# Performance work log

Measured on AMD Instinct MI355X. Metric: run time of the kernel, lower is better.

The kernel has to match this reference:

```python
import jax, jax.numpy as jnp
import numpy as np

C = 768; NUM_HEADS = 12; HID = 3072
HP = 14; WP = 14; TF = 8; BATCH = 4
EPS = 1e-5


def layer_norm(x, g, b):
    mu = jnp.mean(x, axis=-1, keepdims=True)
    var = jnp.mean((x - mu) ** 2, axis=-1, keepdims=True)
    return (x - mu) / jnp.sqrt(var + EPS) * g + b


def mha(x, qkv_w, qkv_b, proj_w, proj_b):
    # Manual multi-head softmax attention, faithful to Attention.forward.
    B, N, Cd = x.shape
    D = Cd // NUM_HEADS
    qkv = (x @ qkv_w.T + qkv_b).reshape(B, N, 3, NUM_HEADS, D).transpose(2, 0, 3, 1, 4)
    q, k, v = qkv[0], qkv[1], qkv[2]  # [B, H, N, D]
    attn = jax.nn.softmax(jnp.einsum('bhnd,bhmd->bhnm', q, k) * (D ** -0.5), axis=-1)
    out = jnp.einsum('bhnm,bhmd->bhnd', attn, v).transpose(0, 2, 1, 3).reshape(B, N, Cd)
    return out @ proj_w.T + proj_b


def setup_inputs() -> dict:
    key = jax.random.key(0)
    ks = jax.random.split(key, 16)
    p = lambda i, s: jax.random.normal(ks[i], s, jnp.float32) * 0.02
    N = 1 + HP * WP * TF  # cls token + spatial*temporal tokens
    return {
        'x': jax.random.normal(ks[0], (BATCH, N, C), jnp.float32),
        'ln_t_g': jnp.ones((C,), jnp.float32), 'ln_t_b': jnp.zeros((C,), jnp.float32),
        't_qkv_w': p(1, (3 * C, C)), 't_qkv_b': p(2, (3 * C,)),
        't_proj_w': p(3, (C, C)), 't_proj_b': p(4, (C,)),
        't_fc_w': p(5, (C, C)), 't_fc_b': p(6, (C,)),
        'ln1_g': jnp.ones((C,), jnp.float32), 'ln1_b': jnp.zeros((C,), jnp.float32),
        's_qkv_w': p(7, (3 * C, C)), 's_qkv_b': p(8, (3 * C,)),
        's_proj_w': p(9, (C, C)), 's_proj_b': p(10, (C,)),
        'ln2_g': jnp.ones((C,), jnp.float32), 'ln2_b': jnp.zeros((C,), jnp.float32),
        'fc1_w': p(11, (HID, C)), 'fc1_b': p(12, (HID,)),
        'fc2_w': p(13, (C, HID)), 'fc2_b': p(14, (C,)),
        'B': BATCH, 'T': TF, 'W': WP,
    }


def reference(x, ln_t_g, ln_t_b, t_qkv_w, t_qkv_b, t_proj_w, t_proj_b, t_fc_w, t_fc_b,
              ln1_g, ln1_b, s_qkv_w, s_qkv_b, s_proj_w, s_proj_b,
              ln2_g, ln2_b, fc1_w, fc1_b, fc2_w, fc2_b, B, T, W):
    # Block.forward, attention_type='divided_space_time', extra_tokens=0, is_cls=True.
    Bv, Ntot, Cd = x.shape
    H = ((Ntot - 1) // T) // W
    # --- temporal attention: 'b (h w t) m -> (b h w) t m' ---
    xt = x[:, 1:, :].reshape(B, H, W, T, Cd).reshape(B * H * W, T, Cd)
    res_t = mha(layer_norm(xt, ln_t_g, ln_t_b), t_qkv_w, t_qkv_b, t_proj_w, t_proj_b)
    res_t = res_t.reshape(B, H * W * T, Cd) @ t_fc_w.T + t_fc_b
    xt = x[:, 1:, :] + res_t  # [B, H*W*T, C]
    # --- spatial attention: 'b (h w t) m -> (b t) (h w) m' with cls token per frame ---
    init_cls = x[:, :1, :]  # [B, 1, C]
    cls_tok = jnp.repeat(init_cls, T, axis=1).reshape(B * T, 1, Cd)
    xs = xt.reshape(B, H, W, T, Cd).transpose(0, 3, 1, 2, 4).reshape(B * T, H * W, Cd)
    xs = jnp.concatenate([cls_tok, xs], axis=1)  # [(B*T), 1+H*W, C]
    res_s = mha(layer_norm(xs, ln1_g, ln1_b), s_qkv_w, s_qkv_b, s_proj_w, s_proj_b)
    cls_out = jnp.mean(res_s[:, 0, :].reshape(B, T, Cd), axis=1, keepdims=True)  # mean over frames
    res_s = res_s[:, 1:, :].reshape(B, T, H, W, Cd).transpose(0, 2, 3, 1, 4).reshape(B, H * W * T, Cd)
    x = jnp.concatenate([init_cls, xt], axis=1) + jnp.concatenate([cls_out, res_s], axis=1)
    # --- MLP (exact GELU, as nn.GELU default) ---
    h = layer_norm(x, ln2_g, ln2_b)
    h = jax.nn.gelu(h @ fc1_w.T + fc1_b, approximate=False)
    return x + (h @ fc2_w.T + fc2_b)
```

## Files before the change

### kernel.cpp

```cpp
#include <hip/hip_runtime.h>
#include <hip/hip_bf16.h>

typedef __bf16 bf16x8 __attribute__((ext_vector_type(8)));
typedef float f32x4 __attribute__((ext_vector_type(4)));
typedef __hip_bfloat16 bf16;

#define NTOK 1569

__device__ __forceinline__ void gl_lds16(const void* g, void* l) {
  __builtin_amdgcn_global_load_lds(
      (const __attribute__((address_space(1))) void*)g,
      (__attribute__((address_space(3))) void*)l, 16, 0, 0);
}

__device__ __forceinline__ unsigned short bf16bits(float v) {
  union { __hip_bfloat16 h; unsigned short u; } cv;
  cv.h = __float2bfloat16(v);
  return cv.u;
}

__global__ void cvt_bf16_k(const float4* __restrict__ src, uint2* __restrict__ dst, int n4) {
  int i = blockIdx.x * 256 + threadIdx.x;
  if (i < n4) {
    float4 v = src[i];
    union { unsigned short h[4]; uint2 u; } pk;
    pk.h[0] = bf16bits(v.x); pk.h[1] = bf16bits(v.y);
    pk.h[2] = bf16bits(v.z); pk.h[3] = bf16bits(v.w);
    dst[i] = pk.u;
  }
}

__global__ void cvt_t_k(const float* __restrict__ src, bf16* __restrict__ dst) {
  int idx = blockIdx.x * 256 + threadIdx.x;
  int r = idx / 768, c = idx % 768;
  dst[(size_t)c * 768 + r] = __float2bfloat16(src[idx]);
}

__global__ __launch_bounds__(256) void bcomb_k(const float* __restrict__ Wf,
                                               const float* __restrict__ bp,
                                               const float* __restrict__ bfv,
                                               float* __restrict__ out) {
  int j = blockIdx.x * 4 + (threadIdx.x >> 6);
  int l = threadIdx.x & 63;
  if (j >= 768) return;
  float s = 0.f;
#pragma unroll
  for (int u = 0; u < 12; ++u) s += Wf[(size_t)j * 768 + l + 64 * u] * bp[l + 64 * u];
#pragma unroll
  for (int o = 1; o < 64; o <<= 1) s += __shfl_xor(s, o);
  if (l == 0) out[j] = s + bfv[j];
}

__global__ __launch_bounds__(256) void ln_k(
    const float* __restrict__ xsrc, const float* __restrict__ xt,
    const float* __restrict__ gam, const float* __restrict__ bet,
    bf16* __restrict__ y, int M, int mode) {
  int r = blockIdx.x * 4 + (threadIdx.x >> 6);
  int l = threadIdx.x & 63;
  if (r >= M) return;
  const float* src;
  if (mode == 0) {
    src = xsrc + (size_t)(r + r / 1568 + 1) * 768;
  } else {
    int g = r / 197, j = r % 197;
    int b = g >> 3, t = g & 7;
    if (j == 0) src = xsrc + (size_t)b * NTOK * 768;
    else        src = xt + (size_t)(b * 1568 + (j - 1) * 8 + t) * 768;
  }
  const float4* s4 = (const float4*)src;
  const float4* g4 = (const float4*)gam;
  const float4* b4 = (const float4*)bet;
  float4 v[3]; float s = 0.f, s2 = 0.f;
#pragma unroll
  for (int u = 0; u < 3; ++u) {
    float4 t4 = s4[l + 64 * u];
    v[u] = t4;
    s += t4.x + t4.y + t4.z + t4.w;
    s2 += t4.x * t4.x + t4.y * t4.y + t4.z * t4.z + t4.w * t4.w;
  }
#pragma unroll
  for (int o = 1; o < 64; o <<= 1) { s += __shfl_xor(s, o); s2 += __shfl_xor(s2, o); }
  float mu = s * (1.f / 768.f);
  float rstd = rsqrtf(s2 * (1.f / 768.f) - mu * mu + 1e-5f);
  uint2* yr = (uint2*)(y + (size_t)r * 768);
#pragma unroll
  for (int u = 0; u < 3; ++u) {
    int j = l + 64 * u;
    float4 gg = g4[j], bb = b4[j];
    union { unsigned short h[4]; uint2 u2; } pk;
    pk.h[0] = bf16bits((v[u].x - mu) * rstd * gg.x + bb.x);
    pk.h[1] = bf16bits((v[u].y - mu) * rstd * gg.y + bb.y);
    pk.h[2] = bf16bits((v[u].z - mu) * rstd * gg.z + bb.z);
    pk.h[3] = bf16bits((v[u].w - mu) * rstd * gg.w + bb.w);
    yr[j] = pk.u2;
  }
}

__global__ __launch_bounds__(256) void combine_ln_k(
    const float* __restrict__ x, const float* __restrict__ xt,
    const float* __restrict__ rs, const float* __restrict__ gam,
    const float* __restrict__ bet, float* __restrict__ xn,
    bf16* __restrict__ y) {
  int r = blockIdx.x * 4 + (threadIdx.x >> 6);
  int l = threadIdx.x & 63;
  if (r >= 4 * NTOK) return;
  int b = r / NTOK, n = r % NTOK;
  float4 v[3]; float s = 0.f, s2 = 0.f;
  if (n == 0) {
#pragma unroll
    for (int u = 0; u < 3; ++u) {
      int j = l + 64 * u;
      float4 a = {0.f, 0.f, 0.f, 0.f};
#pragma unroll
      for (int t = 0; t < 8; ++t) {
        float4 rv = ((const float4*)(rs + (size_t)((b * 8 + t) * 197) * 768))[j];
        a.x += rv.x; a.y += rv.y; a.z += rv.z; a.w += rv.w;
      }
      float4 xv = ((const float4*)(x + (size_t)r * 768))[j];
      v[u].x = xv.x + a.x * 0.125f; v[u].y = xv.y + a.y * 0.125f;
      v[u].z = xv.z + a.z * 0.125f; v[u].w = xv.w + a.w * 0.125f;
    }
  } else {
    int hw = (n - 1) >> 3, t = (n - 1) & 7;
    const float4* xt4 = (const float4*)(xt + (size_t)(b * 1568 + n - 1) * 768);
    const float4* rs4 = (const float4*)(rs + (size_t)((b * 8 + t) * 197 + 1 + hw) * 768);
#pragma unroll
    for (int u = 0; u < 3; ++u) {
      int j = l + 64 * u;
      float4 a = xt4[j], c = rs4[j];
      v[u].x = a.x + c.x; v[u].y = a.y + c.y; v[u].z = a.z + c.z; v[u].w = a.w + c.w;
    }
  }
  float4* xn4 = (float4*)(xn + (size_t)r * 768);
#pragma unroll
  for (int u = 0; u < 3; ++u) {
    xn4[l + 64 * u] = v[u];
    s += v[u].x + v[u].y + v[u].z + v[u].w;
    s2 += v[u].x * v[u].x + v[u].y * v[u].y + v[u].z * v[u].z + v[u].w * v[u].w;
  }
#pragma unroll
  for (int o = 1; o < 64; o <<= 1) { s += __shfl_xor(s, o); s2 += __shfl_xor(s2, o); }
  float mu = s * (1.f / 768.f);
  float rstd = rsqrtf(s2 * (1.f / 768.f) - mu * mu + 1e-5f);
  const float4* g4 = (const float4*)gam;
  const float4* b4 = (const float4*)bet;
  uint2* yr = (uint2*)(y + (size_t)r * 768);
#pragma unroll
  for (int u = 0; u < 3; ++u) {
    int j = l + 64 * u;
    float4 gg = g4[j], bb = b4[j];
    union { unsigned short h[4]; uint2 u2; } pk;
    pk.h[0] = bf16bits((v[u].x - mu) * rstd * gg.x + bb.x);
    pk.h[1] = bf16bits((v[u].y - mu) * rstd * gg.y + bb.y);
    pk.h[2] = bf16bits((v[u].z - mu) * rstd * gg.z + bb.z);
    pk.h[3] = bf16bits((v[u].w - mu) * rstd * gg.w + bb.w);
    yr[j] = pk.u2;
  }
}

template <int OUTBF16, int RES, int GELU>
__global__ __launch_bounds__(256, 3) void gemm_k(
    const bf16* __restrict__ X, const bf16* __restrict__ W,
    const float* __restrict__ bias, const float* __restrict__ resid,
    void* __restrict__ outp, int M, int N, int K) {
  constexpr int BUFB = 256 * 64;
  __shared__ __align__(16) char LDS[3 * BUFB];
  const int tid = threadIdx.x;
  const int w = tid >> 6, l = tid & 63;
  const int wr = w >> 1, wc = w & 1;
  const int lr = l & 15, lg = l >> 4;

  const int nwg = gridDim.x;
  const int orig = blockIdx.x;
  const int qd = nwg >> 3, rm = nwg & 7;
  const int xcd = orig & 7, lot = orig >> 3;
  const int swz = (xcd < rm ? xcd * (qd + 1) : rm * (qd + 1) + (xcd - rm) * qd) + lot;
  const int ntx = N >> 7;
  const int m0 = (swz / ntx) << 7, n0 = (swz % ntx) << 7;

  const char* pA[2]; const char* pB[2]; int dA[2], dB[2];
#pragma unroll
  for (int i = 0; i < 2; ++i) {
    int d = (i * 256 + tid) * 16;
    int s = d ^ (((d >> 7) & 3) << 4);
    int r = s >> 6, cb = s & 63;
    int ga = m0 + r; if (ga >= M) ga = M - 1;
    pA[i] = (const char*)X + (size_t)ga * K * 2 + cb;
    pB[i] = (const char*)W + (size_t)(n0 + r) * K * 2 + (s & 63);
    dA[i] = d; dB[i] = d;
  }

  auto stage = [&](size_t ko, int buf) {
    char* Ab = LDS + buf * BUFB;
    char* Bb = Ab + 128 * 64;
#pragma unroll
    for (int i = 0; i < 2; ++i) gl_lds16(pA[i] + ko, Ab + dA[i]);
#pragma unroll
    for (int i = 0; i < 2; ++i) gl_lds16(pB[i] + ko, Bb + dB[i]);
  };

  f32x4 acc[4][4] = {};
  const int nt = K >> 5;
  stage(0, 0);
  stage(64, 1);
  size_t ko2 = 128;
  int bufS = 2, bufC = 0;
  for (int t = 0; t < nt; ++t) {
    if (t + 2 < nt) {
      stage(ko2, bufS);
      ko2 += 64;
      bufS = (bufS == 2) ? 0 : bufS + 1;
      asm volatile("s_waitcnt vmcnt(8)" ::: "memory");
    } else if (t + 1 < nt) {
      asm volatile("s_waitcnt vmcnt(4)" ::: "memory");
    } else {
      asm volatile("s_waitcnt vmcnt(0)" ::: "memory");
    }
    asm volatile("s_barrier" ::: "memory");
    const char* Ab = LDS + bufC * BUFB;
    const char* Bb = Ab + 128 * 64;
    bufC = (bufC == 2) ? 0 : bufC + 1;
    bf16x8 af[4], bg[4];
#pragma unroll
    for (int mf = 0; mf < 4; ++mf) {
      int d = (wr * 64 + mf * 16 + lr) * 64 + lg * 16;
      af[mf] = *(const bf16x8*)(Ab + (d ^ (((d >> 7) & 3) << 4)));
    }
#pragma unroll
    for (int nf = 0; nf < 4; ++nf) {
      int d = (wc * 64 + nf * 16 + lr) * 64 + lg * 16;
      bg[nf] = *(const bf16x8*)(Bb + (d ^ (((d >> 7) & 3) << 4)));
    }
    __builtin_amdgcn_s_setprio(1);
#pragma unroll
    for (int mf = 0; mf < 4; ++mf)
#pragma unroll
      for (int nf = 0; nf < 4; ++nf)
        acc[mf][nf] = __builtin_amdgcn_mfma_f32_16x16x32_bf16(af[mf], bg[nf], acc[mf][nf], 0, 0, 0);
    __builtin_amdgcn_s_setprio(0);
    asm volatile("s_barrier" ::: "memory");
  }

#pragma unroll
  for (int mf = 0; mf < 4; ++mf) {
    int rowb = m0 + wr * 64 + mf * 16 + lg * 4;
#pragma unroll
    for (int nf = 0; nf < 4; ++nf) {
      int col = n0 + wc * 64 + nf * 16 + lr;
      float bv = bias ? bias[col] : 0.f;
#pragma unroll
      for (int q = 0; q < 4; ++q) {
        int row = rowb + q;
        if (row < M) {
          float v = acc[mf][nf][q] + bv;
          if (GELU) v = 0.5f * v * (1.f + erff(v * 0.70710678118654752f));
          if (RES == 1) v += resid[(size_t)(row + row / 1568 + 1) * 768 + col];
          if (RES == 2) v += resid[(size_t)row * N + col];
          if (OUTBF16) ((bf16*)outp)[(size_t)row * N + col] = __float2bfloat16(v);
          else         ((float*)outp)[(size_t)row * N + col] = v;
        }
      }
    }
  }
}

__global__ __launch_bounds__(256) void attn_t_k(const bf16* __restrict__ qkv,
                                                bf16* __restrict__ outp) {
  __shared__ float sh[4][3 * 520];
  const int wv = threadIdx.x >> 6, l = threadIdx.x & 63;
  const int g = blockIdx.x * 4 + wv;
  const int sq = g / 12, hd = g % 12;
  float* qs = sh[wv];
  float* ks = qs + 520;
  float* vs = qs + 1040;
  const bf16* base = qkv + (size_t)sq * 8 * 2304 + hd * 64;
#pragma unroll
  for (int i = 0; i < 8; ++i) {
    const bf16* rp = base + (size_t)i * 2304;
    qs[i * 65 + l] = __bfloat162float(rp[l]);
    ks[i * 65 + l] = __bfloat162float(rp[768 + l]);
    vs[i * 65 + l] = __bfloat162float(rp[1536 + l]);
  }
  __builtin_amdgcn_wave_barrier();
  const int i = l >> 3, j = l & 7;
  float s = 0.f;
#pragma unroll
  for (int d = 0; d < 64; ++d) s += qs[i * 65 + d] * ks[j * 65 + d];
  s *= 0.125f;
  float m = s;
  m = fmaxf(m, __shfl_xor(m, 1));
  m = fmaxf(m, __shfl_xor(m, 2));
  m = fmaxf(m, __shfl_xor(m, 4));
  float p = __expf(s - m);
  float sum = p;
  sum += __shfl_xor(sum, 1);
  sum += __shfl_xor(sum, 2);
  sum += __shfl_xor(sum, 4);
  p /= sum;
  float pr[8];
#pragma unroll
  for (int jj = 0; jj < 8; ++jj) pr[jj] = __shfl(p, i * 8 + jj);
  bf16* op = outp + (size_t)(sq * 8) * 768 + hd * 64;
#pragma unroll
  for (int u = 0; u < 8; ++u) {
    int c = j + 8 * u;
    float o = 0.f;
#pragma unroll
    for (int jj = 0; jj < 8; ++jj) o += pr[jj] * vs[jj * 65 + c];
    op[(size_t)i * 768 + c] = __float2bfloat16(o);
  }
}

__global__ __launch_bounds__(256) void build_vt_k(const bf16* __restrict__ qkv,
                                                  bf16* __restrict__ vt) {
  const int sq = blockIdx.x / 12, hd = blockIdx.x % 12;
  const bf16* vsrc = qkv + (size_t)sq * 197 * 2304 + 1536 + hd * 64;
  bf16* dst = vt + (size_t)blockIdx.x * 64 * 224;
  for (int idx = threadIdx.x; idx < 197 * 64; idx += 256) {
    int j = idx >> 6, d = idx & 63;
    dst[d * 224 + j] = vsrc[(size_t)j * 2304 + d];
  }
}

__global__ __launch_bounds__(256) void attn_s_k(
    const bf16* __restrict__ qkv, const bf16* __restrict__ vt,
    bf16* __restrict__ outp) {
  __shared__ __align__(16) bf16 P[4][16 * 232];
  const int wv = threadIdx.x >> 6, l = threadIdx.x & 63;
  const int sq = blockIdx.x / 12, hd = blockIdx.x % 12;
  const int lr = l & 15, lg = l >> 4;
  bf16* Pw = P[wv];
#pragma unroll
  for (int idx = 0; idx < 4; ++idx) {
    int e = idx * 64 + l;
    Pw[(e >> 4) * 232 + 208 + (e & 15)] = __float2bfloat16(0.f);
  }
  const bf16* qbase = qkv + (size_t)sq * 197 * 2304 + hd * 64;
  const bf16* kbase = qbase + 768;
  const bf16* vbase = vt + (size_t)blockIdx.x * 64 * 224;
  for (int qt = wv; qt < 13; qt += 4) {
    int q0 = qt * 16;
    int qrow = q0 + lr; if (qrow > 196) qrow = 196;
    bf16x8 qa0 = *(const bf16x8*)(qbase + (size_t)qrow * 2304 + lg * 8);
    bf16x8 qa1 = *(const bf16x8*)(qbase + (size_t)qrow * 2304 + 32 + lg * 8);
    f32x4 sacc[13];
#pragma unroll
    for (int jt = 0; jt < 13; ++jt) {
      const bf16* kp = kbase + (size_t)(jt * 16 + lr) * 2304;
      bf16x8 kb0 = *(const bf16x8*)(kp + lg * 8);
      bf16x8 kb1 = *(const bf16x8*)(kp + 32 + lg * 8);
      f32x4 z = {};
      z = __builtin_amdgcn_mfma_f32_16x16x32_bf16(qa0, kb0, z, 0, 0, 0);
      z = __builtin_amdgcn_mfma_f32_16x16x32_bf16(qa1, kb1, z, 0, 0, 0);
      sacc[jt] = z;
    }
#pragma unroll
    for (int jt = 0; jt < 13; ++jt) {
      bool valid = (jt * 16 + lr) < 197;
#pragma unroll
      for (int q = 0; q < 4; ++q)
        sacc[jt][q] = valid ? sacc[jt][q] * 0.125f : -3e38f;
    }
    float inv[4];
#pragma unroll
    for (int q = 0; q < 4; ++q) {
      float m = -3e38f;
#pragma unroll
      for (int jt = 0; jt < 13; ++jt) m = fmaxf(m, sacc[jt][q]);
      m = fmaxf(m, __shfl_xor(m, 1));
      m = fmaxf(m, __shfl_xor(m, 2));
      m = fmaxf(m, __shfl_xor(m, 4));
      m = fmaxf(m, __shfl_xor(m, 8));
      float ssum = 0.f;
#pragma unroll
      for (int jt = 0; jt < 13; ++jt) {
        float p = __expf(sacc[jt][q] - m);
        sacc[jt][q] = p;
        ssum += p;
      }
      ssum += __shfl_xor(ssum, 1);
      ssum += __shfl_xor(ssum, 2);
      ssum += __shfl_xor(ssum, 4);
      ssum += __shfl_xor(ssum, 8);
      inv[q] = 1.f / ssum;
    }
#pragma unroll
    for (int jt = 0; jt < 13; ++jt)
#pragma unroll
      for (int q = 0; q < 4; ++q)
        Pw[(lg * 4 + q) * 232 + jt * 16 + lr] = __float2bfloat16(sacc[jt][q]);
    __builtin_amdgcn_wave_barrier();
    f32x4 oacc[4] = {};
#pragma unroll
    for (int j7 = 0; j7 < 7; ++j7) {
      bf16x8 pa = *(const bf16x8*)(Pw + lr * 232 + j7 * 32 + lg * 8);
#pragma unroll
      for (int n = 0; n < 4; ++n) {
        bf16x8 vb = *(const bf16x8*)(vbase + (size_t)(n * 16 + lr) * 224 + j7 * 32 + lg * 8);
        oacc[n] = __builtin_amdgcn_mfma_f32_16x16x32_bf16(pa, vb, oacc[n], 0, 0, 0);
      }
    }
    __builtin_amdgcn_wave_barrier();
#pragma unroll
    for (int n = 0; n < 4; ++n)
#pragma unroll
      for (int q = 0; q < 4; ++q) {
        int orow = q0 + lg * 4 + q;
        if (orow < 197)
          outp[(size_t)(sq * 197 + orow) * 768 + hd * 64 + n * 16 + lr] =
              __float2bfloat16(oacc[n][q] * inv[q]);
      }
  }
}

extern "C" void kernel_launch(void* const* d_in, const int* in_sizes, int n_in,
                              void* d_out, int out_size, void* d_ws, size_t ws_size,
                              hipStream_t stream) {
  (void)in_sizes; (void)n_in; (void)out_size; (void)ws_size;
  const float* x        = (const float*)d_in[0];
  const float* ln_t_g   = (const float*)d_in[1];
  const float* ln_t_b   = (const float*)d_in[2];
  const float* t_qkv_w  = (const float*)d_in[3];
  const float* t_qkv_b  = (const float*)d_in[4];
  const float* t_proj_w = (const float*)d_in[5];
  const float* t_proj_b = (const float*)d_in[6];
  const float* t_fc_w   = (const float*)d_in[7];
  const float* t_fc_b   = (const float*)d_in[8];
  const float* ln1_g    = (const float*)d_in[9];
  const float* ln1_b    = (const float*)d_in[10];
  const float* s_qkv_w  = (const float*)d_in[11];
  const float* s_qkv_b  = (const float*)d_in[12];
  const float* s_proj_w = (const float*)d_in[13];
  const float* s_proj_b = (const float*)d_in[14];
  const float* ln2_g    = (const float*)d_in[15];
  const float* ln2_b    = (const float*)d_in[16];
  const float* fc1_w    = (const float*)d_in[17];
  const float* fc1_b    = (const float*)d_in[18];
  const float* fc2_w    = (const float*)d_in[19];
  const float* fc2_b    = (const float*)d_in[20];

  char* ws = (char*)d_ws;
  size_t o = 0;
  auto alloc = [&](size_t bytes) { size_t r = o; o += (bytes + 255) & ~(size_t)255; return r; };
  bf16* wqkvt  = (bf16*)(ws + alloc((size_t)2304 * 768 * 2));
  bf16* wqkvs  = (bf16*)(ws + alloc((size_t)2304 * 768 * 2));
  bf16* wprojs = (bf16*)(ws + alloc((size_t)768 * 768 * 2));
  bf16* wfct   = (bf16*)(ws + alloc((size_t)768 * 768 * 2));
  bf16* wpT    = (bf16*)(ws + alloc((size_t)768 * 768 * 2));
  bf16* wcomb  = (bf16*)(ws + alloc((size_t)768 * 768 * 2));
  float* bcomb = (float*)(ws + alloc((size_t)768 * 4));
  bf16* wfc1   = (bf16*)(ws + alloc((size_t)3072 * 768 * 2));
  bf16* wfc2   = (bf16*)(ws + alloc((size_t)768 * 3072 * 2));
  bf16* ybuf   = (bf16*)(ws + alloc((size_t)6400 * 768 * 2));
  char* big    = ws + alloc((size_t)6400 * 3072 * 2);
  bf16* qkvb   = (bf16*)big;
  bf16* h1     = (bf16*)big;
  bf16* abuf   = (bf16*)(ws + alloc((size_t)6400 * 768 * 2));
  char* slotS  = ws + alloc((size_t)6304 * 768 * 4);
  bf16* vtb    = (bf16*)slotS;
  float* rsb   = (float*)slotS;
  float* xtb   = (float*)(ws + alloc((size_t)6272 * 768 * 4));
  float* xnb   = (float*)(ws + alloc((size_t)6276 * 768 * 4));

  cvt_bf16_k<<<1728, 256, 0, stream>>>((const float4*)t_qkv_w, (uint2*)wqkvt, 442368);
  cvt_bf16_k<<<1728, 256, 0, stream>>>((const float4*)s_qkv_w, (uint2*)wqkvs, 442368);
  cvt_bf16_k<<<576, 256, 0, stream>>>((const float4*)s_proj_w, (uint2*)wprojs, 147456);
  cvt_bf16_k<<<576, 256, 0, stream>>>((const float4*)t_fc_w, (uint2*)wfct, 147456);
  cvt_t_k<<<2304, 256, 0, stream>>>(t_proj_w, wpT);
  cvt_bf16_k<<<2304, 256, 0, stream>>>((const float4*)fc1_w, (uint2*)wfc1, 589824);
  cvt_bf16_k<<<2304, 256, 0, stream>>>((const float4*)fc2_w, (uint2*)wfc2, 589824);
  bcomb_k<<<192, 256, 0, stream>>>(t_fc_w, t_proj_b, t_fc_b, bcomb);
  gemm_k<1, 0, 0><<<36, 256, 0, stream>>>(wfct, wpT, nullptr, nullptr, wcomb, 768, 768, 768);

  ln_k<<<1568, 256, 0, stream>>>(x, nullptr, ln_t_g, ln_t_b, ybuf, 6272, 0);
  gemm_k<1, 0, 0><<<882, 256, 0, stream>>>(ybuf, wqkvt, t_qkv_b, nullptr, qkvb, 6272, 2304, 768);
  attn_t_k<<<2352, 256, 0, stream>>>(qkvb, abuf);
  gemm_k<0, 1, 0><<<294, 256, 0, stream>>>(abuf, wcomb, bcomb, x, xtb, 6272, 768, 768);

  ln_k<<<1576, 256, 0, stream>>>(x, xtb, ln1_g, ln1_b, ybuf, 6304, 1);
  gemm_k<1, 0, 0><<<900, 256, 0, stream>>>(ybuf, wqkvs, s_qkv_b, nullptr, qkvb, 6304, 2304, 768);
  build_vt_k<<<384, 256, 0, stream>>>(qkvb, vtb);
  attn_s_k<<<384, 256, 0, stream>>>(qkvb, vtb, abuf);
  gemm_k<0, 0, 0><<<300, 256, 0, stream>>>(abuf, wprojs, s_proj_b, nullptr, rsb, 6304, 768, 768);

  combine_ln_k<<<1569, 256, 0, stream>>>(x, xtb, rsb, ln2_g, ln2_b, xnb, ybuf);

  gemm_k<1, 0, 1><<<1200, 256, 0, stream>>>(ybuf, wfc1, fc1_b, nullptr, h1, 6276, 3072, 768);
  gemm_k<0, 2, 0><<<300, 256, 0, stream>>>(h1, wfc2, fc2_b, xnb, (float*)d_out, 6276, 768, 3072);
}
```

Baseline: 564.8 us.

## Restructure GEMM pipeline to one barrier per k-step and vectorize temporal attention loads

The GEMM main loop is rewritten with a triple-buffer macro unrolled three times. Each step issues the next stage's async global-to-LDS loads, computes the current buffer, then waits and hits a single barrier, replacing the previous two barriers per iteration. Separately, the temporal attention kernel loads Q/K/V with 16-byte vector reads and stores them as float4 into LDS rows padded to 68 floats, instead of scalar per-element loads. The one-barrier scheme relies on the three-buffer rotation to avoid overwriting a buffer still being read. The stride-68 padding may cause more LDS bank conflicts than stride 65 in the dot-product loop.

```diff
diff --git a/kernel.cpp b/kernel.cpp
--- a/kernel.cpp
+++ b/kernel.cpp
@@ -178,7 +178,7 @@
   const int ntx = N >> 7;
   const int m0 = (swz / ntx) << 7, n0 = (swz % ntx) << 7;
 
-  const char* pA[2]; const char* pB[2]; int dA[2], dB[2];
+  const char* pA[2]; const char* pB[2]; int dd[2];
 #pragma unroll
   for (int i = 0; i < 2; ++i) {
     int d = (i * 256 + tid) * 16;
@@ -186,40 +186,21 @@
     int r = s >> 6, cb = s & 63;
     int ga = m0 + r; if (ga >= M) ga = M - 1;
     pA[i] = (const char*)X + (size_t)ga * K * 2 + cb;
-    pB[i] = (const char*)W + (size_t)(n0 + r) * K * 2 + (s & 63);
-    dA[i] = d; dB[i] = d;
-  }
-
-  auto stage = [&](size_t ko, int buf) {
-    char* Ab = LDS + buf * BUFB;
-    char* Bb = Ab + 128 * 64;
-#pragma unroll
-    for (int i = 0; i < 2; ++i) gl_lds16(pA[i] + ko, Ab + dA[i]);
-#pragma unroll
-    for (int i = 0; i < 2; ++i) gl_lds16(pB[i] + ko, Bb + dB[i]);
+    pB[i] = (const char*)W + (size_t)(n0 + r) * K * 2 + cb;
+    dd[i] = d;
+  }
+
+  auto stage = [&](int t, char* buf) {
+    size_t ko = (size_t)t * 64;
+    gl_lds16(pA[0] + ko, buf + dd[0]);
+    gl_lds16(pA[1] + ko, buf + dd[1]);
+    gl_lds16(pB[0] + ko, buf + 8192 + dd[0]);
+    gl_lds16(pB[1] + ko, buf + 8192 + dd[1]);
   };
 
   f32x4 acc[4][4] = {};
-  const int nt = K >> 5;
-  stage(0, 0);
-  stage(64, 1);
-  size_t ko2 = 128;
-  int bufS = 2, bufC = 0;
-  for (int t = 0; t < nt; ++t) {
-    if (t + 2 < nt) {
-      stage(ko2, bufS);
-      ko2 += 64;
-      bufS = (bufS == 2) ? 0 : bufS + 1;
-      asm volatile("s_waitcnt vmcnt(8)" ::: "memory");
-    } else if (t + 1 < nt) {
-      asm volatile("s_waitcnt vmcnt(4)" ::: "memory");
-    } else {
-      asm volatile("s_waitcnt vmcnt(0)" ::: "memory");
-    }
-    asm volatile("s_barrier" ::: "memory");
-    const char* Ab = LDS + bufC * BUFB;
-    const char* Bb = Ab + 128 * 64;
-    bufC = (bufC == 2) ? 0 : bufC + 1;
+  auto comp = [&](const char* Ab) {
+    const char* Bb = Ab + 8192;
     bf16x8 af[4], bg[4];
 #pragma unroll
     for (int mf = 0; mf < 4; ++mf) {
@@ -238,8 +219,25 @@
       for (int nf = 0; nf < 4; ++nf)
         acc[mf][nf] = __builtin_amdgcn_mfma_f32_16x16x32_bf16(af[mf], bg[nf], acc[mf][nf], 0, 0, 0);
     __builtin_amdgcn_s_setprio(0);
-    asm volatile("s_barrier" ::: "memory");
-  }
+  };
+
+  const int nt = K >> 5;
+  stage(0, LDS);
+  stage(1, LDS + BUFB);
+  asm volatile("s_waitcnt vmcnt(4)\n\ts_barrier" ::: "memory");
+  int t = 0;
+#define GSTEP(BC, BS)                                                                      \
+  {                                                                                        \
+    if (t + 2 < nt) stage(t + 2, LDS + (BS) * BUFB);                                       \
+    comp(LDS + (BC) * BUFB);                                                               \
+    if (t + 2 < nt)                                                                        \
+      asm volatile("s_waitcnt vmcnt(4)\n\ts_barrier" ::: "memory");                        \
+    else if (t + 1 < nt)                                                                   \
+      asm volatile("s_waitcnt vmcnt(0)\n\ts_barrier" ::: "memory");                        \
+    ++t;                                                                                   \
+  }
+  while (t < nt) { GSTEP(0, 2) GSTEP(1, 0) GSTEP(2, 1) }
+#undef GSTEP
 
 #pragma unroll
   for (int mf = 0; mf < 4; ++mf) {
@@ -266,26 +264,39 @@
 
 __global__ __launch_bounds__(256) void attn_t_k(const bf16* __restrict__ qkv,
                                                 bf16* __restrict__ outp) {
-  __shared__ float sh[4][3 * 520];
+  __shared__ float sh[4][3 * 8 * 68];
   const int wv = threadIdx.x >> 6, l = threadIdx.x & 63;
   const int g = blockIdx.x * 4 + wv;
   const int sq = g / 12, hd = g % 12;
   float* qs = sh[wv];
-  float* ks = qs + 520;
-  float* vs = qs + 1040;
+  float* ks = qs + 544;
+  float* vs = qs + 1088;
   const bf16* base = qkv + (size_t)sq * 8 * 2304 + hd * 64;
-#pragma unroll
-  for (int i = 0; i < 8; ++i) {
-    const bf16* rp = base + (size_t)i * 2304;
-    qs[i * 65 + l] = __bfloat162float(rp[l]);
-    ks[i * 65 + l] = __bfloat162float(rp[768 + l]);
-    vs[i * 65 + l] = __bfloat162float(rp[1536 + l]);
+  {
+    int row = l >> 3, c8 = (l & 7) * 8;
+    const bf16* rp = base + (size_t)row * 2304 + c8;
+    bf16x8 qv = *(const bf16x8*)rp;
+    bf16x8 kv = *(const bf16x8*)(rp + 768);
+    bf16x8 vv = *(const bf16x8*)(rp + 1536);
+    float* qd = qs + row * 68 + c8;
+    float* kd = ks + row * 68 + c8;
+    float* vd = vs + row * 68 + c8;
+    float4 a, b;
+    a.x = (float)qv[0]; a.y = (float)qv[1]; a.z = (float)qv[2]; a.w = (float)qv[3];
+    b.x = (float)qv[4]; b.y = (float)qv[5]; b.z = (float)qv[6]; b.w = (float)qv[7];
+    *(float4*)qd = a; *(float4*)(qd + 4) = b;
+    a.x = (float)kv[0]; a.y = (float)kv[1]; a.z = (float)kv[2]; a.w = (float)kv[3];
+    b.x = (float)kv[4]; b.y = (float)kv[5]; b.z = (float)kv[6]; b.w = (float)kv[7];
+    *(float4*)kd = a; *(float4*)(kd + 4) = b;
+    a.x = (float)vv[0]; a.y = (float)vv[1]; a.z = (float)vv[2]; a.w = (float)vv[3];
+    b.x = (float)vv[4]; b.y = (float)vv[5]; b.z = (float)vv[6]; b.w = (float)vv[7];
+    *(float4*)vd = a; *(float4*)(vd + 4) = b;
   }
   __builtin_amdgcn_wave_barrier();
   const int i = l >> 3, j = l & 7;
   float s = 0.f;
 #pragma unroll
-  for (int d = 0; d < 64; ++d) s += qs[i * 65 + d] * ks[j * 65 + d];
+  for (int d = 0; d < 64; ++d) s += qs[i * 68 + d] * ks[j * 68 + d];
   s *= 0.125f;
   float m = s;
   m = fmaxf(m, __shfl_xor(m, 1));
@@ -306,7 +317,7 @@
     int c = j + 8 * u;
     float o = 0.f;
 #pragma unroll
-    for (int jj = 0; jj < 8; ++jj) o += pr[jj] * vs[jj * 65 + c];
+    for (int jj = 0; jj < 8; ++jj) o += pr[jj] * vs[jj * 68 + c];
     op[(size_t)i * 768 + c] = __float2bfloat16(o);
   }
 }
```

After: 565.0 us. Within noise of the previous version (+0.0%).
